# Kernel optimization log

Hardware: AMD Instinct MI355X
Metric: run time of the kernel (lower is better)

The kernel has to match this reference:

```python
import jax, jax.numpy as jnp
import numpy as np

B = 131072
NE, NR, D = 500000, 1000, 128
MARGIN = 1.0
EPS = 1e-6  # torch PairwiseDistance default eps


def setup_inputs() -> dict:
    key = jax.random.key(0)
    ks = jax.random.split(key, 10)
    def triples(k1, k2, k3):
        h = jax.random.randint(k1, (B, 1), 0, NE)
        r = jax.random.randint(k2, (B, 1), 0, NR)
        t = jax.random.randint(k3, (B, 1), 0, NE)
        return jnp.concatenate([h, r, t], axis=1)  # (B, 3)
    posX = triples(ks[0], ks[1], ks[2])
    negX = triples(ks[3], ks[4], ks[5])
    W_e = jax.random.normal(ks[6], (NE, D), dtype=jnp.float32)
    W_ep = jax.random.normal(ks[7], (NE, D), dtype=jnp.float32)
    W_r = jax.random.normal(ks[8], (NR, D), dtype=jnp.float32)
    W_rp = jax.random.normal(ks[9], (NR, D), dtype=jnp.float32)
    return {"posX": posX, "negX": negX, "W_e": W_e, "W_ep": W_ep,
            "W_r": W_r, "W_rp": W_rp}


def _score(X, W_e, W_ep, W_r, W_rp):
    # X: (B, 3) int triples [head, relation, tail]
    h, r, t = X[:, 0], X[:, 1], X[:, 2]
    head, headp = W_e[h], W_ep[h]        # (B, D)
    tail, tailp = W_e[t], W_ep[t]        # (B, D)
    rel, relp = W_r[r], W_rp[r]          # (B, D)
    # Mrh = relp ⊗ headp + I (Em == En), so Mrh @ head = head + relp * (headp·head)
    hm = head + relp * jnp.sum(headp * head, axis=-1, keepdims=True)
    tm = tail + relp * jnp.sum(tailp * tail, axis=-1, keepdims=True)
    diff = hm + rel - tm + EPS
    return jnp.sqrt(jnp.sum(diff * diff, axis=-1))  # L2 pairwise distance


def reference(posX, negX, W_e, W_ep, W_r, W_rp):
    pos = _score(posX, W_e, W_ep, W_r, W_rp)
    neg = _score(negX, W_e, W_ep, W_r, W_rp)
    return jnp.sum(jax.nn.relu(pos - neg + MARGIN)) / posX.shape[0]
```

## Files before the change

### kernel.cpp

```cpp
#include <hip/hip_runtime.h>

#define D 128
#define MARGIN 1.0f
#define EPS 1e-6f

__global__ __launch_bounds__(256, 8) void transd_main(
    const int* __restrict__ posX, const int* __restrict__ negX,
    const float* __restrict__ W_e, const float* __restrict__ W_ep,
    const float* __restrict__ W_r, const float* __restrict__ W_rp,
    float* __restrict__ partial_or_out, int nTriples, int atomicMode)
{
    const int tid  = threadIdx.x;
    const int wid  = tid >> 6;
    const int lane = tid & 63;
    const int l    = lane & 31;
    const bool isNeg = (lane >= 32);
    const int* __restrict__ X = isNeg ? negX : posX;

    const int wavesPerBlock = blockDim.x >> 6;
    const int gw = blockIdx.x * wavesPerBlock + wid;
    const int nw = gridDim.x * wavesPerBlock;

    float acc = 0.0f;

    for (int b = gw; b < nTriples; b += nw) {
        const int h = X[b * 3 + 0];
        const int r = X[b * 3 + 1];
        const int t = X[b * 3 + 2];

        const size_t ho = (size_t)h * D + (size_t)l * 4;
        const size_t to = (size_t)t * D + (size_t)l * 4;
        const size_t ro = (size_t)r * D + (size_t)l * 4;

        const float4 head  = *(const float4*)(W_e  + ho);
        const float4 headp = *(const float4*)(W_ep + ho);
        const float4 tail  = *(const float4*)(W_e  + to);
        const float4 tailp = *(const float4*)(W_ep + to);
        const float4 rel   = *(const float4*)(W_r  + ro);
        const float4 relp  = *(const float4*)(W_rp + ro);

        float dh = headp.x * head.x + headp.y * head.y + headp.z * head.z + headp.w * head.w;
        float dt = tailp.x * tail.x + tailp.y * tail.y + tailp.z * tail.z + tailp.w * tail.w;

        #pragma unroll
        for (int m = 1; m <= 16; m <<= 1) {
            dh += __shfl_xor(dh, m, 64);
            dt += __shfl_xor(dt, m, 64);
        }
        const float dd = dh - dt;

        float4 diff;
        diff.x = fmaf(relp.x, dd, head.x - tail.x + rel.x + EPS);
        diff.y = fmaf(relp.y, dd, head.y - tail.y + rel.y + EPS);
        diff.z = fmaf(relp.z, dd, head.z - tail.z + rel.z + EPS);
        diff.w = fmaf(relp.w, dd, head.w - tail.w + rel.w + EPS);

        float ss = diff.x * diff.x + diff.y * diff.y + diff.z * diff.z + diff.w * diff.w;
        #pragma unroll
        for (int m = 1; m <= 16; m <<= 1) ss += __shfl_xor(ss, m, 64);

        const float score = sqrtf(ss);
        const float other = __shfl_xor(score, 32, 64);

        if (lane == 0) acc += fmaxf(0.0f, score - other + MARGIN);
    }

    __shared__ float sacc[8];
    if (lane == 0) sacc[wid] = acc;
    __syncthreads();
    if (tid == 0) {
        float s = 0.0f;
        for (int i = 0; i < wavesPerBlock; ++i) s += sacc[i];
        if (atomicMode) {
            atomicAdd(partial_or_out, s / (float)nTriples);
        } else {
            partial_or_out[blockIdx.x] = s;
        }
    }
}

__global__ void transd_reduce(const float* __restrict__ partial, int n,
                              float* __restrict__ out, int nTriples)
{
    __shared__ float s[256];
    float v = 0.0f;
    for (int i = threadIdx.x; i < n; i += 256) v += partial[i];
    s[threadIdx.x] = v;
    __syncthreads();
    for (int k = 128; k > 0; k >>= 1) {
        if ((int)threadIdx.x < k) s[threadIdx.x] += s[threadIdx.x + k];
        __syncthreads();
    }
    if (threadIdx.x == 0) out[0] = s[0] / (float)nTriples;
}

extern "C" void kernel_launch(void* const* d_in, const int* in_sizes, int n_in,
                              void* d_out, int out_size, void* d_ws, size_t ws_size,
                              hipStream_t stream) {
    const int*   posX = (const int*)d_in[0];
    const int*   negX = (const int*)d_in[1];
    const float* W_e  = (const float*)d_in[2];
    const float* W_ep = (const float*)d_in[3];
    const float* W_r  = (const float*)d_in[4];
    const float* W_rp = (const float*)d_in[5];
    float* out = (float*)d_out;

    const int nTriples = in_sizes[0] / 3;
    const int NB = 2048;

    if (ws_size >= (size_t)NB * sizeof(float)) {
        float* partial = (float*)d_ws;
        hipLaunchKernelGGL(transd_main, dim3(NB), dim3(256), 0, stream,
                           posX, negX, W_e, W_ep, W_r, W_rp, partial, nTriples, 0);
        hipLaunchKernelGGL(transd_reduce, dim3(1), dim3(256), 0, stream,
                           partial, NB, out, nTriples);
    } else {
        hipMemsetAsync(out, 0, sizeof(float), stream);
        hipLaunchKernelGGL(transd_main, dim3(NB), dim3(256), 0, stream,
                           posX, negX, W_e, W_ep, W_r, W_rp, out, nTriples, 1);
    }
}
```

Measured before the change: 96.21 us.

## Fuse final reduction via last-block counter and prefetch next triple indices

Replaces the separate reduce kernel with a last-block-done pattern: each block publishes its partial with a release store, increments a global counter, and the final block performs the 2048-element reduction. It also software-prefetches the next iteration's index triple so index loads overlap with the gather of the current one. This removes one kernel launch but adds a memset launch and an atomic per block. It also drops the fallback path for small workspaces.

```diff
diff --git a/kernel.cpp b/kernel.cpp
--- a/kernel.cpp
+++ b/kernel.cpp
@@ -3,34 +3,45 @@
 #define D 128
 #define MARGIN 1.0f
 #define EPS 1e-6f
+#define NB 2048
+#define WPB 4
 
-__global__ __launch_bounds__(256, 8) void transd_main(
+__global__ __launch_bounds__(256, 8) void transd_fused(
     const int* __restrict__ posX, const int* __restrict__ negX,
     const float* __restrict__ W_e, const float* __restrict__ W_ep,
     const float* __restrict__ W_r, const float* __restrict__ W_rp,
-    float* __restrict__ partial_or_out, int nTriples, int atomicMode)
+    float* __restrict__ partials, unsigned int* __restrict__ counter,
+    float* __restrict__ out, int nTriples)
 {
     const int tid  = threadIdx.x;
     const int wid  = tid >> 6;
     const int lane = tid & 63;
-    const int l    = lane & 31;
-    const bool isNeg = (lane >= 32);
-    const int* __restrict__ X = isNeg ? negX : posX;
+    const int l4   = (lane & 31) * 4;
+    const int* __restrict__ X = (lane >= 32) ? negX : posX;
 
-    const int wavesPerBlock = blockDim.x >> 6;
-    const int gw = blockIdx.x * wavesPerBlock + wid;
-    const int nw = gridDim.x * wavesPerBlock;
+    const int gw = blockIdx.x * WPB + wid;
+    const int nw = NB * WPB;
+
+    const int iters = (gw < nTriples) ? ((nTriples - 1 - gw) / nw + 1) : 0;
 
     float acc = 0.0f;
 
-    for (int b = gw; b < nTriples; b += nw) {
-        const int h = X[b * 3 + 0];
-        const int r = X[b * 3 + 1];
-        const int t = X[b * 3 + 2];
+    int h = 0, r = 0, t = 0;
+    if (iters > 0) {
+        const int b0 = gw;
+        h = X[b0 * 3 + 0]; r = X[b0 * 3 + 1]; t = X[b0 * 3 + 2];
+    }
 
-        const size_t ho = (size_t)h * D + (size_t)l * 4;
-        const size_t to = (size_t)t * D + (size_t)l * 4;
-        const size_t ro = (size_t)r * D + (size_t)l * 4;
+    for (int i = 0; i < iters; ++i) {
+        int nh = h, nr = r, nt = t;
+        if (i + 1 < iters) {
+            const int nb = gw + (i + 1) * nw;
+            nh = X[nb * 3 + 0]; nr = X[nb * 3 + 1]; nt = X[nb * 3 + 2];
+        }
+
+        const size_t ho = (size_t)h * D + l4;
+        const size_t to = (size_t)t * D + l4;
+        const size_t ro = (size_t)r * D + l4;
 
         const float4 head  = *(const float4*)(W_e  + ho);
         const float4 headp = *(const float4*)(W_ep + ho);
@@ -63,35 +74,42 @@
         const float other = __shfl_xor(score, 32, 64);
 
         if (lane == 0) acc += fmaxf(0.0f, score - other + MARGIN);
+
+        h = nh; r = nr; t = nt;
     }
 
-    __shared__ float sacc[8];
+    __shared__ float sacc[WPB];
+    __shared__ int   isLast;
     if (lane == 0) sacc[wid] = acc;
     __syncthreads();
+
     if (tid == 0) {
         float s = 0.0f;
-        for (int i = 0; i < wavesPerBlock; ++i) s += sacc[i];
-        if (atomicMode) {
-            atomicAdd(partial_or_out, s / (float)nTriples);
-        } else {
-            partial_or_out[blockIdx.x] = s;
+        #pragma unroll
+        for (int i = 0; i < WPB; ++i) s += sacc[i];
+        __hip_atomic_store(&partials[blockIdx.x], s,
+                           __ATOMIC_RELEASE, __HIP_MEMORY_SCOPE_AGENT);
+        unsigned int old = __hip_atomic_fetch_add(counter, 1u,
+                           __ATOMIC_ACQ_REL, __HIP_MEMORY_SCOPE_AGENT);
+        isLast = (old == (unsigned)(NB - 1));
+    }
+    __syncthreads();
+
+    if (isLast) {
+        __shared__ float red[256];
+        float v = 0.0f;
+        for (int i = tid; i < NB; i += 256)
+            v += __hip_atomic_load(&partials[i],
+                                   __ATOMIC_RELAXED, __HIP_MEMORY_SCOPE_AGENT);
+        red[tid] = v;
+        __syncthreads();
+        #pragma unroll
+        for (int k = 128; k > 0; k >>= 1) {
+            if (tid < k) red[tid] += red[tid + k];
+            __syncthreads();
         }
+        if (tid == 0) out[0] = red[0] / (float)nTriples;
     }
-}
-
-__global__ void transd_reduce(const float* __restrict__ partial, int n,
-                              float* __restrict__ out, int nTriples)
-{
-    __shared__ float s[256];
-    float v = 0.0f;
-    for (int i = threadIdx.x; i < n; i += 256) v += partial[i];
-    s[threadIdx.x] = v;
-    __syncthreads();
-    for (int k = 128; k > 0; k >>= 1) {
-        if ((int)threadIdx.x < k) s[threadIdx.x] += s[threadIdx.x + k];
-        __syncthreads();
-    }
-    if (threadIdx.x == 0) out[0] = s[0] / (float)nTriples;
 }
 
 extern "C" void kernel_launch(void* const* d_in, const int* in_sizes, int n_in,
@@ -106,17 +124,13 @@
     float* out = (float*)d_out;
 
     const int nTriples = in_sizes[0] / 3;
-    const int NB = 2048;
 
-    if (ws_size >= (size_t)NB * sizeof(float)) {
-        float* partial = (float*)d_ws;
-        hipLaunchKernelGGL(transd_main, dim3(NB), dim3(256), 0, stream,
-                           posX, negX, W_e, W_ep, W_r, W_rp, partial, nTriples, 0);
-        hipLaunchKernelGGL(transd_reduce, dim3(1), dim3(256), 0, stream,
-                           partial, NB, out, nTriples);
-    } else {
-        hipMemsetAsync(out, 0, sizeof(float), stream);
-        hipLaunchKernelGGL(transd_main, dim3(NB), dim3(256), 0, stream,
-                           posX, negX, W_e, W_ep, W_r, W_rp, out, nTriples, 1);
-    }
+    float*        partials = (float*)d_ws;
+    unsigned int* counter  = (unsigned int*)((char*)d_ws + NB * sizeof(float));
+
+    hipMemsetAsync(counter, 0, sizeof(unsigned int), stream);
+
+    hipLaunchKernelGGL(transd_fused, dim3(NB), dim3(256), 0, stream,
+                       posX, negX, W_e, W_ep, W_r, W_rp,
+                       partials, counter, out, nTriples);
 }
```

Measured after the change: 266.0 us. +176.5%, slower.
